# Kernel optimization log

Measured on AMD Instinct MI355X. Metric: run time of the kernel, lower is better.

Reference implementation:

```python
import jax, jax.numpy as jnp
import numpy as np

KS = 3          # deform conv kernel size
N = KS * KS     # sampling points per output pixel
PAD = 1         # zero padding


def _conv3x3(x, w, b):
    out = jax.lax.conv_general_dilated(x, w, (1, 1), ((PAD, PAD), (PAD, PAD)),
                                       dimension_numbers=('NCHW', 'OIHW', 'NCHW'))
    return out + b[None, :, None, None]


def _deform_conv(x, w_p, b_p, w_dc):
    # x: [B,C,H,W]; w_p: [2N,C,3,3]; w_dc: [O,C,3,3]
    B, C, H, W = x.shape
    off = jnp.transpose(_conv3x3(x, w_p, b_p), (0, 2, 3, 1))  # [B,H,W,2N]
    k = jnp.arange(KS, dtype=x.dtype) - (KS - 1) // 2
    pny, pnx = jnp.meshgrid(k, k, indexing='ij')              # kernel grid, row-major
    # base grid starts at 1 because of the zero padding of 1 (stride=1)
    py = jnp.arange(1, H + 1, dtype=x.dtype)[:, None, None] + pny.reshape(-1) + off[..., :N]
    px = jnp.arange(1, W + 1, dtype=x.dtype)[None, :, None] + pnx.reshape(-1) + off[..., N:]
    xp = jnp.pad(x, ((0, 0), (0, 0), (PAD, PAD), (PAD, PAD)))
    Hp, Wp = H + 2 * PAD, W + 2 * PAD
    fy = jnp.floor(jax.lax.stop_gradient(py))
    fx = jnp.floor(jax.lax.stop_gradient(px))
    y0 = jnp.clip(fy, 0, Hp - 1).astype(jnp.int32)
    y1 = jnp.clip(fy + 1, 0, Hp - 1).astype(jnp.int32)
    x0 = jnp.clip(fx, 0, Wp - 1).astype(jnp.int32)
    x1 = jnp.clip(fx + 1, 0, Wp - 1).astype(jnp.int32)
    pyc = jnp.clip(py, 0, Hp - 1)
    pxc = jnp.clip(px, 0, Wp - 1)
    y0f, y1f, x0f, x1f = (a.astype(x.dtype) for a in (y0, y1, x0, x1))
    g_lt = (1 + (y0f - pyc)) * (1 + (x0f - pxc))
    g_rb = (1 - (y1f - pyc)) * (1 - (x1f - pxc))
    g_lb = (1 + (y0f - pyc)) * (1 - (x1f - pxc))
    g_rt = (1 - (y1f - pyc)) * (1 + (x0f - pxc))
    # per-batch gather: [C,Hp,Wp] indexed by [H,W,N] -> [C,H,W,N]
    gat = jax.vmap(lambda im, iy, ix: im[:, iy, ix])
    x_off = (g_lt[:, None] * gat(xp, y0, x0) + g_rb[:, None] * gat(xp, y1, x1)
             + g_lb[:, None] * gat(xp, y0, x1) + g_rt[:, None] * gat(xp, y1, x0))  # [B,C,H,W,N]
    O = w_dc.shape[0]
    # equivalent to reshaping x_off to [B,C,H*KS,W*KS] and conv with stride KS
    return jnp.einsum('bchwn,ocn->bohw', x_off, w_dc.reshape(O, C, N))


def setup_inputs() -> dict:
    key = jax.random.key(0)
    ks = jax.random.split(key, 6)
    B, C, H, W = 4, 2, 2048, 128
    rgb = jax.random.normal(ks[0], (B, C, H, W), jnp.float32)
    sar = jax.random.normal(ks[1], (B, C, H, W), jnp.float32)
    w_fm = jax.random.normal(ks[2], (C, C), jnp.float32) * 0.5   # fsm_fm 1x1, no bias
    w_fs = jax.random.normal(ks[3], (C, C), jnp.float32) * 0.5   # fsm_fs 1x1, no bias
    w_p = jax.random.normal(ks[4], (2 * N, 2 * C, KS, KS), jnp.float32) * 0.05  # offset conv
    b_p = jnp.zeros((2 * N,), jnp.float32)
    w_dc = jax.random.normal(ks[5], (C, 2 * C, KS, KS), jnp.float32) * 0.2      # deform kernel
    return {"rgb": rgb, "sar": sar, "w_fm": w_fm, "w_fs": w_fs,
            "w_p": w_p, "b_p": b_p, "w_dc": w_dc}


def reference(rgb, sar, w_fm, w_fs, w_p, b_p, w_dc):
    B, C, H, W = rgb.shape
    P = 128
    # AdaptiveAvgPool2d((128,128)) with H,W divisible by 128 = exact block mean
    avg = rgb.reshape(B, C, P, H // P, P, W // P).mean(axis=(3, 5))   # [B,C,128,128]
    fm = jax.nn.sigmoid(jnp.einsum('oc,bchw->bohw', w_fm, avg))       # [B,C,128,128]
    mat = jnp.einsum('bchk,bckw->bchw', rgb, fm) + rgb                # rgb.matmul(fm) + rgb
    fs = jnp.einsum('oc,bchw->bohw', w_fs, mat)
    x = jnp.concatenate([sar, fs], axis=1)                            # [B,2C,H,W]
    return _deform_conv(x, w_p, b_p, w_dc)
```

## Files before the change

kernel.cpp:

```cpp
#include <hip/hip_runtime.h>
#include <math.h>

typedef __attribute__((ext_vector_type(2))) _Float16 half2v;
typedef __attribute__((ext_vector_type(2))) float f32x2;
typedef __attribute__((ext_vector_type(4), aligned(8))) unsigned int uint4a;

#define BB 4
#define HH 2048
#define WW 128
#define HP (HH + 2)
#define WP (WW + 2)
#define PP 128
#define MROWS 8

#define BORDER_PER_B (2 * WP + 2 * (HP - 2))

__device__ __forceinline__ half2v b2h(unsigned u) { return __builtin_bit_cast(half2v, u); }
__device__ __forceinline__ unsigned pku(float a, float b) {
    return __builtin_bit_cast(unsigned, __builtin_amdgcn_cvt_pkrtz(a, b));
}
__device__ __forceinline__ float dot2(half2v a, unsigned wb, float c) {
    return __builtin_amdgcn_fdot2(a, b2h(wb), c, false);
}
__device__ __forceinline__ float hlo(unsigned u) { return (float)b2h(u).x; }
__device__ __forceinline__ float hhi(unsigned u) { return (float)b2h(u).y; }


__global__ void k_fm(const float* __restrict__ rgb, const float* __restrict__ w_fm,
                     float2* __restrict__ fmp, uint2* __restrict__ xph) {
    int j = threadIdx.x;
    int bi = blockIdx.x;
    int tid = bi * 128 + j;

    if (tid < BB * BORDER_PER_B) {
        int b = tid / BORDER_PER_B;
        int r = tid - b * BORDER_PER_B;
        int row, col;
        if (r < WP)          { row = 0;      col = r; }
        else if (r < 2 * WP) { row = HP - 1; col = r - WP; }
        else {
            int q = r - 2 * WP;
            row = 1 + (q >> 1);
            col = (q & 1) ? (WP - 1) : 0;
        }
        xph[((size_t)b * HP + row) * WP + col] = make_uint2(0u, 0u);
    }

    int b = bi >> 6, t = bi & 63;
    const float* r0 = rgb + ((size_t)(b * 2 + 0) * HH + (size_t)t * 32) * WW + j;
    const float* r1 = rgb + ((size_t)(b * 2 + 1) * HH + (size_t)t * 32) * WW + j;
    float sA0 = 0.f, sA1 = 0.f, sB0 = 0.f, sB1 = 0.f;
#pragma unroll
    for (int a = 0; a < 16; ++a) { sA0 += r0[a * WW]; sA1 += r1[a * WW]; }
#pragma unroll
    for (int a = 16; a < 32; ++a) { sB0 += r0[a * WW]; sB1 += r1[a * WW]; }
    sA0 *= (1.f / 16.f); sA1 *= (1.f / 16.f);
    sB0 *= (1.f / 16.f); sB1 *= (1.f / 16.f);
    float fA0 = w_fm[0] * sA0 + w_fm[1] * sA1;
    float fA1 = w_fm[2] * sA0 + w_fm[3] * sA1;
    float fB0 = w_fm[0] * sB0 + w_fm[1] * sB1;
    float fB1 = w_fm[2] * sB0 + w_fm[3] * sB1;
    float gA0 = 1.f / (1.f + expf(-fA0)), gB0 = 1.f / (1.f + expf(-fB0));
    float gA1 = 1.f / (1.f + expf(-fA1)), gB1 = 1.f / (1.f + expf(-fB1));
    fmp[((size_t)(b * 2 + 0) * 64 + t) * PP + j] = make_float2(gA0, gB0);
    fmp[((size_t)(b * 2 + 1) * 64 + t) * PP + j] = make_float2(gA1, gB1);
}

__global__ __launch_bounds__(128) void k_mat(
        const float* __restrict__ rgb, const float* __restrict__ sar,
        const float* __restrict__ w_fs, const float2* __restrict__ fmp,
        uint2* __restrict__ xph) {
    int w = threadIdx.x;
    int bid = blockIdx.x;
    int swz = (bid & 7) * 128 + (bid >> 3);
    int b = swz >> 8;
    int h0 = (swz & 255) * 8;

    const float* rg0 = rgb + ((size_t)(b * 2 + 0) * HH + h0) * WW;
    const float* rg1 = rgb + ((size_t)(b * 2 + 1) * HH + h0) * WW;
    const float2* fp0 = fmp + (size_t)(b * 2 + 0) * 64 * PP;
    const float2* fp1 = fmp + (size_t)(b * 2 + 1) * 64 * PP;

    f32x2 av0[MROWS], av1[MROWS];
#pragma unroll
    for (int r = 0; r < MROWS; ++r) {
        av0[r] = (f32x2){rg0[r * WW + w], 0.f};
        av1[r] = (f32x2){rg1[r * WW + w], 0.f};
    }

#pragma unroll 4
    for (int t = 0; t < 64; ++t) {
        float2 f0 = fp0[(size_t)t * PP + w];
        float2 f1 = fp1[(size_t)t * PP + w];
        f32x2 fv0 = {f0.x, f0.y};
        f32x2 fv1 = {f1.x, f1.y};
#pragma unroll
        for (int r = 0; r < MROWS; ++r) {
            f32x2 a0 = *(const f32x2*)(rg0 + r * WW + 2 * t);
            f32x2 a1 = *(const f32x2*)(rg1 + r * WW + 2 * t);
            av0[r] += a0 * fv0;
            av1[r] += a1 * fv1;
        }
    }

    float wa = w_fs[0], wb = w_fs[1], wc = w_fs[2], wd = w_fs[3];
#pragma unroll
    for (int r = 0; r < MROWS; ++r) {
        float m0 = av0[r].x + av0[r].y;
        float m1 = av1[r].x + av1[r].y;
        float fs0 = wa * m0 + wb * m1;
        float fs1 = wc * m0 + wd * m1;
        float s0 = sar[((size_t)(b * 2 + 0) * HH + (h0 + r)) * WW + w];
        float s1 = sar[((size_t)(b * 2 + 1) * HH + (h0 + r)) * WW + w];
        uint2 cell = make_uint2(pku(s0, s1), pku(fs0, fs1));
        xph[((size_t)b * HP + (h0 + r + 1)) * WP + (w + 1)] = cell;
    }
}

__global__ __launch_bounds__(128) void k_deform(
        const float* __restrict__ w_p, const float* __restrict__ b_p,
        const float* __restrict__ w_dc, const uint2* __restrict__ xph,
        float* __restrict__ out) {
    int bid = blockIdx.x;
    int swz = (bid & 7) * 512 + (bid >> 3);
    int b = swz >> 10;
    int h = (swz & 1023) * 2;
    int w = threadIdx.x;

    const uint2* xb = xph + (size_t)b * HP * WP;
    const unsigned* xbu = (const unsigned*)xb;
    float* outb = out + (size_t)(b * 2) * HH * WW;

    uint2 nbc[4][3];
#pragma unroll
    for (int dy = 0; dy < 4; ++dy)
#pragma unroll
        for (int dx = 0; dx < 3; ++dx)
            nbc[dy][dx] = xb[(h + dy) * WP + (w + dx)];

    f32x2 prs[3][3][4];
#pragma unroll
    for (int ky = 0; ky < 3; ++ky)
#pragma unroll
        for (int kx = 0; kx < 3; ++kx) {
            uint2 cA = nbc[ky][kx], cB = nbc[ky + 1][kx];
            prs[ky][kx][0] = (f32x2){hlo(cA.x), hlo(cB.x)};
            prs[ky][kx][1] = (f32x2){hhi(cA.x), hhi(cB.x)};
            prs[ky][kx][2] = (f32x2){hlo(cA.y), hlo(cB.y)};
            prs[ky][kx][3] = (f32x2){hhi(cA.y), hhi(cB.y)};
        }

    f32x2 off2[18];
#pragma unroll
    for (int r = 0; r < 18; ++r) {
        float bias = b_p[r];
        f32x2 s = (f32x2){bias, bias};
#pragma unroll
        for (int ky = 0; ky < 3; ++ky)
#pragma unroll
            for (int kx = 0; kx < 3; ++kx) {
                const float* wr = w_p + r * 36 + ky * 3 + kx;
                s += wr[0] * prs[ky][kx][0] + wr[9] * prs[ky][kx][1]
                   + wr[18] * prs[ky][kx][2] + wr[27] * prs[ky][kx][3];
            }
        off2[r] = s;
    }

    float acc0[2] = {0.f, 0.f};
    float acc1[2] = {0.f, 0.f};

#pragma unroll
    for (int g = 0; g < 3; ++g) {
        unsigned hg[3][2][4];
        bool adj[3][2];
        uint4a q0[3][2], q1[3][2];

#pragma unroll
        for (int j = 0; j < 3; ++j) {
            int n = g * 3 + j;
            int pny = n / 3 - 1;
            int pnx = n % 3 - 1;
            f32x2 py2 = (f32x2){(float)(h + 1 + pny), (float)(h + 2 + pny)} + off2[n];
            f32x2 px2 = (float)(w + 1 + pnx) + off2[9 + n];
            f32x2 fy2 = {floorf(py2.x), floorf(py2.y)};
            f32x2 fx2 = {floorf(px2.x), floorf(px2.y)};
            f32x2 y0f = {fminf(fmaxf(fy2.x, 0.f), (float)(HP - 1)),
                         fminf(fmaxf(fy2.y, 0.f), (float)(HP - 1))};
            f32x2 y1f = {fminf(fmaxf(fy2.x + 1.f, 0.f), (float)(HP - 1)),
                         fminf(fmaxf(fy2.y + 1.f, 0.f), (float)(HP - 1))};
            f32x2 x0f = {fminf(fmaxf(fx2.x, 0.f), (float)(WP - 1)),
                         fminf(fmaxf(fx2.y, 0.f), (float)(WP - 1))};
            f32x2 x1f = {fminf(fmaxf(fx2.x + 1.f, 0.f), (float)(WP - 1)),
                         fminf(fmaxf(fx2.y + 1.f, 0.f), (float)(WP - 1))};
            f32x2 pyc = {fminf(fmaxf(py2.x, 0.f), (float)(HP - 1)),
                         fminf(fmaxf(py2.y, 0.f), (float)(HP - 1))};
            f32x2 pxc = {fminf(fmaxf(px2.x, 0.f), (float)(WP - 1)),
                         fminf(fmaxf(px2.y, 0.f), (float)(WP - 1))};
            f32x2 ay = 1.f + (y0f - pyc);
            f32x2 by = 1.f - (y1f - pyc);
            f32x2 ax = 1.f + (x0f - pxc);
            f32x2 bx = 1.f - (x1f - pxc);
            f32x2 glt = ay * ax, grb = by * bx, glb = ay * bx, grt = by * ax;

#pragma unroll
            for (int p = 0; p < 2; ++p) {
                int y0 = (int)(p ? y0f.y : y0f.x);
                int y1 = (int)(p ? y1f.y : y1f.x);
                int x0 = (int)(p ? x0f.y : x0f.x);
                int x1 = (int)(p ? x1f.y : x1f.x);
                float g_lt = p ? glt.y : glt.x;
                float g_rb = p ? grb.y : grb.x;
                float g_lb = p ? glb.y : glb.x;
                float g_rt = p ? grt.y : grt.x;
                hg[j][p][0] = pku(g_lt, g_lt);
                hg[j][p][1] = pku(g_rb, g_rb);
                hg[j][p][2] = pku(g_lb, g_lb);
                hg[j][p][3] = pku(g_rt, g_rt);
                adj[j][p] = (x1 > x0);
                q0[j][p] = *(const uint4a*)(xbu + 2 * (y0 * WP + x0));
                q1[j][p] = *(const uint4a*)(xbu + 2 * (y1 * WP + x0));
            }
        }

#pragma unroll
        for (int j = 0; j < 3; ++j) {
            int n = g * 3 + j;
            unsigned wd00 = pku(w_dc[0 * 36 + 0 * 9 + n], w_dc[0 * 36 + 1 * 9 + n]);
            unsigned wd01 = pku(w_dc[0 * 36 + 2 * 9 + n], w_dc[0 * 36 + 3 * 9 + n]);
            unsigned wd10 = pku(w_dc[1 * 36 + 0 * 9 + n], w_dc[1 * 36 + 1 * 9 + n]);
            unsigned wd11 = pku(w_dc[1 * 36 + 2 * 9 + n], w_dc[1 * 36 + 3 * 9 + n]);
#pragma unroll
            for (int p = 0; p < 2; ++p) {
                uint4a a = q0[j][p], c = q1[j][p];
                bool ad = adj[j][p];
                unsigned lt01 = a.x, lt23 = a.y;
                unsigned lb01 = ad ? a.z : a.x, lb23 = ad ? a.w : a.y;
                unsigned rt01 = c.x, rt23 = c.y;
                unsigned rb01 = ad ? c.z : c.x, rb23 = ad ? c.w : c.y;

                half2v h01 = b2h(hg[j][p][0]) * b2h(lt01) + b2h(hg[j][p][1]) * b2h(rb01)
                           + b2h(hg[j][p][2]) * b2h(lb01) + b2h(hg[j][p][3]) * b2h(rt01);
                half2v h23 = b2h(hg[j][p][0]) * b2h(lt23) + b2h(hg[j][p][1]) * b2h(rb23)
                           + b2h(hg[j][p][2]) * b2h(lb23) + b2h(hg[j][p][3]) * b2h(rt23);

                acc0[p] = dot2(h01, wd00, acc0[p]);
                acc0[p] = dot2(h23, wd01, acc0[p]);
                acc1[p] = dot2(h01, wd10, acc1[p]);
                acc1[p] = dot2(h23, wd11, acc1[p]);
            }
        }
    }
#pragma unroll
    for (int p = 0; p < 2; ++p) {
        outb[(h + p) * WW + w] = acc0[p];
        outb[HH * WW + (h + p) * WW + w] = acc1[p];
    }
}

extern "C" void kernel_launch(void* const* d_in, const int* in_sizes, int n_in,
                              void* d_out, int out_size, void* d_ws, size_t ws_size,
                              hipStream_t stream) {
    const float* rgb  = (const float*)d_in[0];
    const float* sar  = (const float*)d_in[1];
    const float* w_fm = (const float*)d_in[2];
    const float* w_fs = (const float*)d_in[3];
    const float* w_p  = (const float*)d_in[4];
    const float* b_p  = (const float*)d_in[5];
    const float* w_dc = (const float*)d_in[6];
    float* out = (float*)d_out;

    float* ws = (float*)d_ws;
    float2* fmp = (float2*)ws;
    uint2* xph = (uint2*)(ws + 131072);

    k_fm<<<BB * 64, 128, 0, stream>>>(rgb, w_fm, fmp, xph);
    k_mat<<<BB * (HH / MROWS), 128, 0, stream>>>(rgb, sar, w_fs, fmp, xph);
    k_deform<<<BB * (HH / 2), 128, 0, stream>>>(w_p, b_p, w_dc, xph, out);
}
```

Before: 56.02 us.

## Split deform kernel into offset-conv and sampling kernels via workspace buffer

Replaces the single fused deform kernel with two kernels. The first computes the 18 offset channels and stores them as packed fp16 in a workspace buffer, and the second reads those offsets and does the bilinear sampling plus the deform-conv reduction. The aim is to lower register pressure and raise occupancy in each kernel. The cost is an extra launch and a round trip of about 9 MB of offsets through global memory. The fused kernel is kept as a fallback when the workspace is too small.

```diff
diff --git a/kernel.cpp b/kernel.cpp
--- a/kernel.cpp
+++ b/kernel.cpp
@@ -12,6 +12,7 @@
 #define WP (WW + 2)
 #define PP 128
 #define MROWS 8
+#define NPX (BB * HH * WW / 2)
 
 #define BORDER_PER_B (2 * WP + 2 * (HP - 2))
 
@@ -114,6 +115,172 @@
         float s1 = sar[((size_t)(b * 2 + 1) * HH + (h0 + r)) * WW + w];
         uint2 cell = make_uint2(pku(s0, s1), pku(fs0, fs1));
         xph[((size_t)b * HP + (h0 + r + 1)) * WP + (w + 1)] = cell;
+    }
+}
+
+__global__ __launch_bounds__(128) void k_off(
+        const float* __restrict__ w_p, const float* __restrict__ b_p,
+        const uint2* __restrict__ xph, unsigned* __restrict__ offb) {
+    int bid = blockIdx.x;
+    int swz = (bid & 7) * 512 + (bid >> 3);
+    int b = swz >> 10;
+    int h = (swz & 1023) * 2;
+    int w = threadIdx.x;
+
+    const uint2* xb = xph + (size_t)b * HP * WP;
+
+    uint2 nbc[4][3];
+#pragma unroll
+    for (int dy = 0; dy < 4; ++dy)
+#pragma unroll
+        for (int dx = 0; dx < 3; ++dx)
+            nbc[dy][dx] = xb[(h + dy) * WP + (w + dx)];
+
+    f32x2 prs[3][3][4];
+#pragma unroll
+    for (int ky = 0; ky < 3; ++ky)
+#pragma unroll
+        for (int kx = 0; kx < 3; ++kx) {
+            uint2 cA = nbc[ky][kx], cB = nbc[ky + 1][kx];
+            prs[ky][kx][0] = (f32x2){hlo(cA.x), hlo(cB.x)};
+            prs[ky][kx][1] = (f32x2){hhi(cA.x), hhi(cB.x)};
+            prs[ky][kx][2] = (f32x2){hlo(cA.y), hlo(cB.y)};
+            prs[ky][kx][3] = (f32x2){hhi(cA.y), hhi(cB.y)};
+        }
+
+    f32x2 off2[18];
+#pragma unroll
+    for (int r = 0; r < 18; ++r) {
+        float bias = b_p[r];
+        f32x2 s = (f32x2){bias, bias};
+#pragma unroll
+        for (int ky = 0; ky < 3; ++ky)
+#pragma unroll
+            for (int kx = 0; kx < 3; ++kx) {
+                const float* wr = w_p + r * 36 + ky * 3 + kx;
+                s += wr[0] * prs[ky][kx][0] + wr[9] * prs[ky][kx][1]
+                   + wr[18] * prs[ky][kx][2] + wr[27] * prs[ky][kx][3];
+            }
+        off2[r] = s;
+    }
+
+    int gid = bid * 128 + w;
+#pragma unroll
+    for (int n = 0; n < 9; ++n) {
+        offb[(size_t)(2 * n + 0) * NPX + gid] = pku(off2[n].x, off2[n + 9].x);
+        offb[(size_t)(2 * n + 1) * NPX + gid] = pku(off2[n].y, off2[n + 9].y);
+    }
+}
+
+__global__ __launch_bounds__(128) void k_samp(
+        const float* __restrict__ w_dc, const uint2* __restrict__ xph,
+        const unsigned* __restrict__ offb, float* __restrict__ out) {
+    int bid = blockIdx.x;
+    int swz = (bid & 7) * 512 + (bid >> 3);
+    int b = swz >> 10;
+    int h = (swz & 1023) * 2;
+    int w = threadIdx.x;
+
+    const uint2* xb = xph + (size_t)b * HP * WP;
+    const unsigned* xbu = (const unsigned*)xb;
+    float* outb = out + (size_t)(b * 2) * HH * WW;
+
+    int gid = bid * 128 + w;
+    unsigned uo[18];
+#pragma unroll
+    for (int k = 0; k < 18; ++k)
+        uo[k] = offb[(size_t)k * NPX + gid];
+
+    float acc0[2] = {0.f, 0.f};
+    float acc1[2] = {0.f, 0.f};
+
+#pragma unroll
+    for (int g = 0; g < 3; ++g) {
+        unsigned hg[3][2][4];
+        bool adj[3][2];
+        uint4a q0[3][2], q1[3][2];
+
+#pragma unroll
+        for (int j = 0; j < 3; ++j) {
+            int n = g * 3 + j;
+            int pny = n / 3 - 1;
+            int pnx = n % 3 - 1;
+            f32x2 offy = {hlo(uo[2 * n]), hlo(uo[2 * n + 1])};
+            f32x2 offx = {hhi(uo[2 * n]), hhi(uo[2 * n + 1])};
+            f32x2 py2 = (f32x2){(float)(h + 1 + pny), (float)(h + 2 + pny)} + offy;
+            f32x2 px2 = (float)(w + 1 + pnx) + offx;
+            f32x2 fy2 = {floorf(py2.x), floorf(py2.y)};
+            f32x2 fx2 = {floorf(px2.x), floorf(px2.y)};
+            f32x2 y0f = {fminf(fmaxf(fy2.x, 0.f), (float)(HP - 1)),
+                         fminf(fmaxf(fy2.y, 0.f), (float)(HP - 1))};
+            f32x2 y1f = {fminf(fmaxf(fy2.x + 1.f, 0.f), (float)(HP - 1)),
+                         fminf(fmaxf(fy2.y + 1.f, 0.f), (float)(HP - 1))};
+            f32x2 x0f = {fminf(fmaxf(fx2.x, 0.f), (float)(WP - 1)),
+                         fminf(fmaxf(fx2.y, 0.f), (float)(WP - 1))};
+            f32x2 x1f = {fminf(fmaxf(fx2.x + 1.f, 0.f), (float)(WP - 1)),
+                         fminf(fmaxf(fx2.y + 1.f, 0.f), (float)(WP - 1))};
+            f32x2 pyc = {fminf(fmaxf(py2.x, 0.f), (float)(HP - 1)),
+                         fminf(fmaxf(py2.y, 0.f), (float)(HP - 1))};
+            f32x2 pxc = {fminf(fmaxf(px2.x, 0.f), (float)(WP - 1)),
+                         fminf(fmaxf(px2.y, 0.f), (float)(WP - 1))};
+            f32x2 ay = 1.f + (y0f - pyc);
+            f32x2 by = 1.f - (y1f - pyc);
+            f32x2 ax = 1.f + (x0f - pxc);
+            f32x2 bx = 1.f - (x1f - pxc);
+            f32x2 glt = ay * ax, grb = by * bx, glb = ay * bx, grt = by * ax;
+
+#pragma unroll
+            for (int p = 0; p < 2; ++p) {
+                int y0 = (int)(p ? y0f.y : y0f.x);
+                int y1 = (int)(p ? y1f.y : y1f.x);
+                int x0 = (int)(p ? x0f.y : x0f.x);
+                int x1 = (int)(p ? x1f.y : x1f.x);
+                float g_lt = p ? glt.y : glt.x;
+                float g_rb = p ? grb.y : grb.x;
+                float g_lb = p ? glb.y : glb.x;
+                float g_rt = p ? grt.y : grt.x;
+                hg[j][p][0] = pku(g_lt, g_lt);
+                hg[j][p][1] = pku(g_rb, g_rb);
+                hg[j][p][2] = pku(g_lb, g_lb);
+                hg[j][p][3] = pku(g_rt, g_rt);
+                adj[j][p] = (x1 > x0);
+                q0[j][p] = *(const uint4a*)(xbu + 2 * (y0 * WP + x0));
+                q1[j][p] = *(const uint4a*)(xbu + 2 * (y1 * WP + x0));
+            }
+        }
+
+#pragma unroll
+        for (int j = 0; j < 3; ++j) {
+            int n = g * 3 + j;
+            unsigned wd00 = pku(w_dc[0 * 36 + 0 * 9 + n], w_dc[0 * 36 + 1 * 9 + n]);
+            unsigned wd01 = pku(w_dc[0 * 36 + 2 * 9 + n], w_dc[0 * 36 + 3 * 9 + n]);
+            unsigned wd10 = pku(w_dc[1 * 36 + 0 * 9 + n], w_dc[1 * 36 + 1 * 9 + n]);
+            unsigned wd11 = pku(w_dc[1 * 36 + 2 * 9 + n], w_dc[1 * 36 + 3 * 9 + n]);
+#pragma unroll
+            for (int p = 0; p < 2; ++p) {
+                uint4a a = q0[j][p], c = q1[j][p];
+                bool ad = adj[j][p];
+                unsigned lt01 = a.x, lt23 = a.y;
+                unsigned lb01 = ad ? a.z : a.x, lb23 = ad ? a.w : a.y;
+                unsigned rt01 = c.x, rt23 = c.y;
+                unsigned rb01 = ad ? c.z : c.x, rb23 = ad ? c.w : c.y;
+
+                half2v h01 = b2h(hg[j][p][0]) * b2h(lt01) + b2h(hg[j][p][1]) * b2h(rb01)
+                           + b2h(hg[j][p][2]) * b2h(lb01) + b2h(hg[j][p][3]) * b2h(rt01);
+                half2v h23 = b2h(hg[j][p][0]) * b2h(lt23) + b2h(hg[j][p][1]) * b2h(rb23)
+                           + b2h(hg[j][p][2]) * b2h(lb23) + b2h(hg[j][p][3]) * b2h(rt23);
+
+                acc0[p] = dot2(h01, wd00, acc0[p]);
+                acc0[p] = dot2(h23, wd01, acc0[p]);
+                acc1[p] = dot2(h01, wd10, acc1[p]);
+                acc1[p] = dot2(h23, wd11, acc1[p]);
+            }
+        }
+    }
+#pragma unroll
+    for (int p = 0; p < 2; ++p) {
+        outb[(h + p) * WW + w] = acc0[p];
+        outb[HH * WW + (h + p) * WW + w] = acc1[p];
     }
 }
 
@@ -272,8 +439,16 @@
     float* ws = (float*)d_ws;
     float2* fmp = (float2*)ws;
     uint2* xph = (uint2*)(ws + 131072);
+    unsigned* offb = (unsigned*)(xph + (size_t)BB * HP * WP);
+    size_t need = (size_t)131072 * 4 + (size_t)BB * HP * WP * 8
+                + (size_t)18 * NPX * 4;
 
     k_fm<<<BB * 64, 128, 0, stream>>>(rgb, w_fm, fmp, xph);
     k_mat<<<BB * (HH / MROWS), 128, 0, stream>>>(rgb, sar, w_fs, fmp, xph);
-    k_deform<<<BB * (HH / 2), 128, 0, stream>>>(w_p, b_p, w_dc, xph, out);
-}
+    if (ws_size >= need) {
+        k_off<<<BB * (HH / 2), 128, 0, stream>>>(w_p, b_p, xph, offb);
+        k_samp<<<BB * (HH / 2), 128, 0, stream>>>(w_dc, xph, offb, out);
+    } else {
+        k_deform<<<BB * (HH / 2), 128, 0, stream>>>(w_p, b_p, w_dc, xph, out);
+    }
+}
```

New measurement: 67.31 us. 1.2x slower.

## Fuse offset conv into rolled per-point loop to cut register pressure

Applied to the files above, without the earlier changes.

Replaces the precomputed 18-entry offset array and fully unrolled 3x3 sampling groups with a rolled loop over the nine sampling points. Each iteration computes its own y/x offset pair, then samples and accumulates at once. It also adds a minimum-blocks hint of 4 to launch bounds. The aim is fewer live registers and higher occupancy, at the cost of less memory-level parallelism, since gather loads are no longer batched three points at a time, plus some loop overhead.

```diff
diff --git a/kernel.cpp b/kernel.cpp
--- a/kernel.cpp
+++ b/kernel.cpp
@@ -117,7 +117,7 @@
     }
 }
 
-__global__ __launch_bounds__(128) void k_deform(
+__global__ __launch_bounds__(128, 4) void k_deform(
         const float* __restrict__ w_p, const float* __restrict__ b_p,
         const float* __restrict__ w_dc, const uint2* __restrict__ xph,
         float* __restrict__ out) {
@@ -150,106 +150,93 @@
             prs[ky][kx][3] = (f32x2){hhi(cA.y), hhi(cB.y)};
         }
 
-    f32x2 off2[18];
-#pragma unroll
-    for (int r = 0; r < 18; ++r) {
-        float bias = b_p[r];
-        f32x2 s = (f32x2){bias, bias};
-#pragma unroll
-        for (int ky = 0; ky < 3; ++ky)
-#pragma unroll
-            for (int kx = 0; kx < 3; ++kx) {
-                const float* wr = w_p + r * 36 + ky * 3 + kx;
-                s += wr[0] * prs[ky][kx][0] + wr[9] * prs[ky][kx][1]
-                   + wr[18] * prs[ky][kx][2] + wr[27] * prs[ky][kx][3];
-            }
-        off2[r] = s;
-    }
-
     float acc0[2] = {0.f, 0.f};
     float acc1[2] = {0.f, 0.f};
 
-#pragma unroll
-    for (int g = 0; g < 3; ++g) {
-        unsigned hg[3][2][4];
-        bool adj[3][2];
-        uint4a q0[3][2], q1[3][2];
-
-#pragma unroll
-        for (int j = 0; j < 3; ++j) {
-            int n = g * 3 + j;
-            int pny = n / 3 - 1;
-            int pnx = n % 3 - 1;
-            f32x2 py2 = (f32x2){(float)(h + 1 + pny), (float)(h + 2 + pny)} + off2[n];
-            f32x2 px2 = (float)(w + 1 + pnx) + off2[9 + n];
-            f32x2 fy2 = {floorf(py2.x), floorf(py2.y)};
-            f32x2 fx2 = {floorf(px2.x), floorf(px2.y)};
-            f32x2 y0f = {fminf(fmaxf(fy2.x, 0.f), (float)(HP - 1)),
-                         fminf(fmaxf(fy2.y, 0.f), (float)(HP - 1))};
-            f32x2 y1f = {fminf(fmaxf(fy2.x + 1.f, 0.f), (float)(HP - 1)),
-                         fminf(fmaxf(fy2.y + 1.f, 0.f), (float)(HP - 1))};
-            f32x2 x0f = {fminf(fmaxf(fx2.x, 0.f), (float)(WP - 1)),
-                         fminf(fmaxf(fx2.y, 0.f), (float)(WP - 1))};
-            f32x2 x1f = {fminf(fmaxf(fx2.x + 1.f, 0.f), (float)(WP - 1)),
-                         fminf(fmaxf(fx2.y + 1.f, 0.f), (float)(WP - 1))};
-            f32x2 pyc = {fminf(fmaxf(py2.x, 0.f), (float)(HP - 1)),
-                         fminf(fmaxf(py2.y, 0.f), (float)(HP - 1))};
-            f32x2 pxc = {fminf(fmaxf(px2.x, 0.f), (float)(WP - 1)),
-                         fminf(fmaxf(px2.y, 0.f), (float)(WP - 1))};
-            f32x2 ay = 1.f + (y0f - pyc);
-            f32x2 by = 1.f - (y1f - pyc);
-            f32x2 ax = 1.f + (x0f - pxc);
-            f32x2 bx = 1.f - (x1f - pxc);
-            f32x2 glt = ay * ax, grb = by * bx, glb = ay * bx, grt = by * ax;
-
-#pragma unroll
-            for (int p = 0; p < 2; ++p) {
-                int y0 = (int)(p ? y0f.y : y0f.x);
-                int y1 = (int)(p ? y1f.y : y1f.x);
-                int x0 = (int)(p ? x0f.y : x0f.x);
-                int x1 = (int)(p ? x1f.y : x1f.x);
-                float g_lt = p ? glt.y : glt.x;
-                float g_rb = p ? grb.y : grb.x;
-                float g_lb = p ? glb.y : glb.x;
-                float g_rt = p ? grt.y : grt.x;
-                hg[j][p][0] = pku(g_lt, g_lt);
-                hg[j][p][1] = pku(g_rb, g_rb);
-                hg[j][p][2] = pku(g_lb, g_lb);
-                hg[j][p][3] = pku(g_rt, g_rt);
-                adj[j][p] = (x1 > x0);
-                q0[j][p] = *(const uint4a*)(xbu + 2 * (y0 * WP + x0));
-                q1[j][p] = *(const uint4a*)(xbu + 2 * (y1 * WP + x0));
+#pragma unroll 1
+    for (int n = 0; n < 9; ++n) {
+        int pny = n / 3 - 1;
+        int pnx = n % 3 - 1;
+
+        const float* wrA = w_p + n * 36;
+        const float* wrB = w_p + (9 + n) * 36;
+        f32x2 offy = {b_p[n], b_p[n]};
+        f32x2 offx = {b_p[9 + n], b_p[9 + n]};
+#pragma unroll
+        for (int ky = 0; ky < 3; ++ky)
+#pragma unroll
+            for (int kx = 0; kx < 3; ++kx) {
+                int t = ky * 3 + kx;
+#pragma unroll
+                for (int c = 0; c < 4; ++c) {
+                    offy += wrA[c * 9 + t] * prs[ky][kx][c];
+                    offx += wrB[c * 9 + t] * prs[ky][kx][c];
+                }
             }
-        }
-
-#pragma unroll
-        for (int j = 0; j < 3; ++j) {
-            int n = g * 3 + j;
-            unsigned wd00 = pku(w_dc[0 * 36 + 0 * 9 + n], w_dc[0 * 36 + 1 * 9 + n]);
-            unsigned wd01 = pku(w_dc[0 * 36 + 2 * 9 + n], w_dc[0 * 36 + 3 * 9 + n]);
-            unsigned wd10 = pku(w_dc[1 * 36 + 0 * 9 + n], w_dc[1 * 36 + 1 * 9 + n]);
-            unsigned wd11 = pku(w_dc[1 * 36 + 2 * 9 + n], w_dc[1 * 36 + 3 * 9 + n]);
-#pragma unroll
-            for (int p = 0; p < 2; ++p) {
-                uint4a a = q0[j][p], c = q1[j][p];
-                bool ad = adj[j][p];
-                unsigned lt01 = a.x, lt23 = a.y;
-                unsigned lb01 = ad ? a.z : a.x, lb23 = ad ? a.w : a.y;
-                unsigned rt01 = c.x, rt23 = c.y;
-                unsigned rb01 = ad ? c.z : c.x, rb23 = ad ? c.w : c.y;
-
-                half2v h01 = b2h(hg[j][p][0]) * b2h(lt01) + b2h(hg[j][p][1]) * b2h(rb01)
-                           + b2h(hg[j][p][2]) * b2h(lb01) + b2h(hg[j][p][3]) * b2h(rt01);
-                half2v h23 = b2h(hg[j][p][0]) * b2h(lt23) + b2h(hg[j][p][1]) * b2h(rb23)
-                           + b2h(hg[j][p][2]) * b2h(lb23) + b2h(hg[j][p][3]) * b2h(rt23);
-
-                acc0[p] = dot2(h01, wd00, acc0[p]);
-                acc0[p] = dot2(h23, wd01, acc0[p]);
-                acc1[p] = dot2(h01, wd10, acc1[p]);
-                acc1[p] = dot2(h23, wd11, acc1[p]);
-            }
-        }
-    }
+
+        f32x2 py2 = (f32x2){(float)(h + 1 + pny), (float)(h + 2 + pny)} + offy;
+        f32x2 px2 = (float)(w + 1 + pnx) + offx;
+        f32x2 fy2 = {floorf(py2.x), floorf(py2.y)};
+        f32x2 fx2 = {floorf(px2.x), floorf(px2.y)};
+        f32x2 y0f = {fminf(fmaxf(fy2.x, 0.f), (float)(HP - 1)),
+                     fminf(fmaxf(fy2.y, 0.f), (float)(HP - 1))};
+        f32x2 y1f = {fminf(fmaxf(fy2.x + 1.f, 0.f), (float)(HP - 1)),
+                     fminf(fmaxf(fy2.y + 1.f, 0.f), (float)(HP - 1))};
+        f32x2 x0f = {fminf(fmaxf(fx2.x, 0.f), (float)(WP - 1)),
+                     fminf(fmaxf(fx2.y, 0.f), (float)(WP - 1))};
+        f32x2 x1f = {fminf(fmaxf(fx2.x + 1.f, 0.f), (float)(WP - 1)),
+                     fminf(fmaxf(fx2.y + 1.f, 0.f), (float)(WP - 1))};
+        f32x2 pyc = {fminf(fmaxf(py2.x, 0.f), (float)(HP - 1)),
+                     fminf(fmaxf(py2.y, 0.f), (float)(HP - 1))};
+        f32x2 pxc = {fminf(fmaxf(px2.x, 0.f), (float)(WP - 1)),
+                     fminf(fmaxf(px2.y, 0.f), (float)(WP - 1))};
+        f32x2 ay = 1.f + (y0f - pyc);
+        f32x2 by = 1.f - (y1f - pyc);
+        f32x2 ax = 1.f + (x0f - pxc);
+        f32x2 bx = 1.f - (x1f - pxc);
+        f32x2 glt = ay * ax, grb = by * bx, glb = ay * bx, grt = by * ax;
+
+        unsigned wd00 = pku(w_dc[0 * 36 + 0 * 9 + n], w_dc[0 * 36 + 1 * 9 + n]);
+        unsigned wd01 = pku(w_dc[0 * 36 + 2 * 9 + n], w_dc[0 * 36 + 3 * 9 + n]);
+        unsigned wd10 = pku(w_dc[1 * 36 + 0 * 9 + n], w_dc[1 * 36 + 1 * 9 + n]);
+        unsigned wd11 = pku(w_dc[1 * 36 + 2 * 9 + n], w_dc[1 * 36 + 3 * 9 + n]);
+
+#pragma unroll
+        for (int p = 0; p < 2; ++p) {
+            int y0 = (int)(p ? y0f.y : y0f.x);
+            int y1 = (int)(p ? y1f.y : y1f.x);
+            int x0 = (int)(p ? x0f.y : x0f.x);
+            int x1 = (int)(p ? x1f.y : x1f.x);
+            float g_lt = p ? glt.y : glt.x;
+            float g_rb = p ? grb.y : grb.x;
+            float g_lb = p ? glb.y : glb.x;
+            float g_rt = p ? grt.y : grt.x;
+
+            uint4a q0 = *(const uint4a*)(xbu + 2 * (y0 * WP + x0));
+            uint4a q1 = *(const uint4a*)(xbu + 2 * (y1 * WP + x0));
+            bool ad = (x1 > x0);
+            unsigned lt01 = q0.x, lt23 = q0.y;
+            unsigned lb01 = ad ? q0.z : q0.x, lb23 = ad ? q0.w : q0.y;
+            unsigned rt01 = q1.x, rt23 = q1.y;
+            unsigned rb01 = ad ? q1.z : q1.x, rb23 = ad ? q1.w : q1.y;
+
+            unsigned hlt = pku(g_lt, g_lt);
+            unsigned hrb = pku(g_rb, g_rb);
+            unsigned hlb = pku(g_lb, g_lb);
+            unsigned hrt = pku(g_rt, g_rt);
+
+            half2v h01 = b2h(hlt) * b2h(lt01) + b2h(hrb) * b2h(rb01)
+                       + b2h(hlb) * b2h(lb01) + b2h(hrt) * b2h(rt01);
+            half2v h23 = b2h(hlt) * b2h(lt23) + b2h(hrb) * b2h(rb23)
+                       + b2h(hlb) * b2h(lb23) + b2h(hrt) * b2h(rt23);
+
+            acc0[p] = dot2(h01, wd00, acc0[p]);
+            acc0[p] = dot2(h23, wd01, acc0[p]);
+            acc1[p] = dot2(h01, wd10, acc1[p]);
+            acc1[p] = dot2(h23, wd11, acc1[p]);
+        }
+    }
+
 #pragma unroll
     for (int p = 0; p < 2; ++p) {
         outb[(h + p) * WW + w] = acc0[p];
```

New measurement: 53.85 us, median of 2. 1.04x faster.
